# Performance work log

Measured on AMD Instinct MI355X. Metric: run time of the kernel, lower is better.

The kernel has to match this reference:

```python
import math
import jax, jax.numpy as jnp
import numpy as np

Bn, NA, NE = 16384, 15, 16
H, NH, DH = 256, 4, 64
DO, DA, DE = 30, 32, 32
NACT, BS = 6, 2048


def setup_inputs():
    key = jax.random.key(0)
    c = [0]
    def nxt():
        c[0] += 1
        return jax.random.fold_in(key, c[0])
    def nrm(shape, scale=1.0):
        return jax.random.normal(nxt(), shape, jnp.float32) * scale
    sH = 1.0 / math.sqrt(H)
    own_raw = nrm((Bn, 1, DO))
    ally_raw = nrm((Bn, NA, DA))
    enemy_raw = nrm((Bn, NE, DE))
    # zero-rows encode invisible entities (mask is derived from all-zero check)
    mA = jax.random.bernoulli(nxt(), 0.8, (Bn, NA)).at[:, 0].set(True)
    mE = jax.random.bernoulli(nxt(), 0.8, (Bn, NE)).at[:, 0].set(True)
    ally_raw = ally_raw * mA[..., None]
    enemy_raw = enemy_raw * mE[..., None]
    return dict(
        own_raw=own_raw, ally_raw=ally_raw, enemy_raw=enemy_raw,
        hidden_state=nrm((Bn, H), 0.1),
        W_own=nrm((H, DO), 1.0 / math.sqrt(DO)), b_own=jnp.zeros((H,)),
        W_ally=nrm((H, DA), 1.0 / math.sqrt(DA)), b_ally=jnp.zeros((H,)),
        W_enemy=nrm((H, DE), 1.0 / math.sqrt(DE)), b_enemy=jnp.zeros((H,)),
        gt_w=nrm((2,), 0.1), gt_b=jnp.zeros((2,)),
        attnA_W=nrm((4, H, H), sH), attnA_b=jnp.zeros((4, H)),
        attnE_W=nrm((4, H, H), sH), attnE_b=jnp.zeros((4, H)),
        clnA_W=nrm((2, H, H), 0.1 * sH), clnA_b=jnp.zeros((2, H)),
        clnE_W=nrm((2, H, H), 0.1 * sH), clnE_b=jnp.zeros((2, H)),
        ln3_g=jnp.ones((3 * H,)), ln3_b=jnp.zeros((3 * H,)),
        gru_Wih=nrm((3 * H, 3 * H), 1.0 / math.sqrt(3 * H)),
        gru_Whh=nrm((3 * H, H), sH),
        gru_bih=jnp.zeros((3 * H,)), gru_bhh=jnp.zeros((3 * H,)),
        Wv_head=nrm((1, H), sH), bv_head=jnp.zeros((1,)),
        Wtb=nrm((2, H), sH), btb=jnp.zeros((2,)),
        log_tau=jnp.zeros((2,)),
        Wmq=nrm((H, H), sH), bmq=jnp.zeros((H,)),
        prototypes=nrm((NACT, H), sH),
        Wqs=nrm((H, H), sH), bqs=jnp.zeros((H,)),
        Wke=nrm((H, H), sH), bke=jnp.zeros((H,)),
        bs=BS,
    )


def _group_temp(cnt, w, b):
    # GroupTemp: positive temperature from group cardinality
    return jax.nn.softplus(w * jnp.log1p(cnt) + b) + 1.0


def _mhga(q, K, mask, temp, W, b):
    # multi-head group attention: single query over a small entity set
    B, N, _ = K.shape
    qh = (q @ W[0].T + b[0]).reshape(B, NH, DH)
    kh = (K @ W[1].T + b[1]).reshape(B, N, NH, DH)
    vh = (K @ W[2].T + b[2]).reshape(B, N, NH, DH)
    s = jnp.einsum('bhd,bnhd->bhn', qh, kh) / math.sqrt(DH)
    s = s / temp[:, None, None]
    s = jnp.where(mask[:, None, :], s, -1e30)
    p = jax.nn.softmax(s, axis=-1)
    z = jnp.einsum('bhn,bnhd->bhd', p, vh).reshape(B, H)
    return z @ W[3].T + b[3]


def _cln(x, cond, W, b, eps=1e-5):
    # conditional LayerNorm: scale/shift predicted from own-feature embedding
    mu = x.mean(-1, keepdims=True)
    var = ((x - mu) ** 2).mean(-1, keepdims=True)
    xn = (x - mu) * jax.lax.rsqrt(var + eps)
    gamma = 1.0 + cond @ W[0].T + b[0]
    beta = cond @ W[1].T + b[1]
    return gamma * xn + beta


def _ln(x, g, b, eps=1e-5):
    mu = x.mean(-1, keepdims=True)
    var = ((x - mu) ** 2).mean(-1, keepdims=True)
    return (x - mu) * jax.lax.rsqrt(var + eps) * g + b


def reference(own_raw, ally_raw, enemy_raw, hidden_state, W_own, b_own,
              W_ally, b_ally, W_enemy, b_enemy, gt_w, gt_b,
              attnA_W, attnA_b, attnE_W, attnE_b,
              clnA_W, clnA_b, clnE_W, clnE_b, ln3_g, ln3_b,
              gru_Wih, gru_Whh, gru_bih, gru_bhh,
              Wv_head, bv_head, Wtb, btb, log_tau,
              Wmq, bmq, prototypes, Wqs, bqs, Wke, bke, bs):
    ally_mask = jnp.any(ally_raw != 0, axis=-1)     # [B,nA]
    enemy_mask = jnp.any(enemy_raw != 0, axis=-1)   # [B,nE]
    e_own = own_raw @ W_own.T + b_own               # [B,1,H]
    A = ally_raw @ W_ally.T + b_ally                # [B,nA,H]
    E = enemy_raw @ W_enemy.T + b_enemy             # [B,nE,H]
    q_src = e_own[:, 0]
    tA = _group_temp(ally_mask.sum(-1).astype(jnp.float32), gt_w[0], gt_b[0])
    tE = _group_temp(enemy_mask.sum(-1).astype(jnp.float32), gt_w[1], gt_b[1])
    zA = _cln(_mhga(q_src, A, ally_mask, tA, attnA_W, attnA_b), q_src, clnA_W, clnA_b)
    zE = _cln(_mhga(q_src, E, enemy_mask, tE, attnE_W, attnE_b), q_src, clnE_W, clnE_b)
    u = _ln(jnp.concatenate([q_src, zA, zE], axis=-1), ln3_g, ln3_b)
    # GRUCell (PyTorch gate layout: r, z, n)
    gi = u @ gru_Wih.T + gru_bih
    gh = hidden_state @ gru_Whh.T + gru_bhh
    ir, iz, inn = jnp.split(gi, 3, axis=-1)
    hr, hz, hn = jnp.split(gh, 3, axis=-1)
    r = jax.nn.sigmoid(ir + hr)
    zg = jax.nn.sigmoid(iz + hz)
    n = jnp.tanh(inn + r * hn)
    h = (1.0 - zg) * n + zg * hidden_state
    V = h @ Wv_head.T + bv_head                     # [B,1]
    tb = h @ Wtb.T + btb
    b_move, b_shoot = tb[:, 0:1], tb[:, 1:2]
    tau_move = jnp.exp(log_tau[0]) + 1e-6
    tau_shoot = jnp.exp(log_tau[1]) + 1e-6
    # prototype movement head
    q_mv = h @ Wmq.T + bmq
    A_move = q_mv @ prototypes.T / math.sqrt(H)
    A_move = A_move - A_move.mean(-1, keepdims=True)
    Q_move = V + b_move + A_move / tau_move
    # shoot pointer head over enemies
    q_sh = h @ Wqs.T + bqs
    Ke = E @ Wke.T + bke
    a = jnp.einsum('bh,bnh->bn', q_sh, Ke) / math.sqrt(H)
    emf = enemy_mask.astype(a.dtype)
    den = jnp.maximum(emf.sum(1, keepdims=True), 1.0)
    a = a - (a * emf).sum(1, keepdims=True) / den
    a = jnp.where(enemy_mask, a, -1e30)
    Q_shoot = V + b_shoot + a / tau_shoot
    Q = jnp.concatenate([Q_move, Q_shoot], axis=-1)[:, None, :]  # [B,1,NACT+nE]
    return Q, h.reshape(bs, -1, H)
```

## Files before the change

kernel.cpp:

```cpp
#include <hip/hip_runtime.h>
#include <math.h>

#define BN 16384

typedef float f32x4 __attribute__((ext_vector_type(4)));
typedef short bf16x8v __attribute__((ext_vector_type(8)));
typedef unsigned short u16x8 __attribute__((ext_vector_type(8)));
typedef unsigned short u16x4 __attribute__((ext_vector_type(4)));

static __device__ inline unsigned short f2bf(float f) {
  unsigned u = __float_as_uint(f);
  return (unsigned short)((u + 0x8000u) >> 16);
}
static __device__ inline float bf2f(unsigned short u) {
  return __uint_as_float(((unsigned)u) << 16);
}

#define XS(r) (((r) >> 1) & 3)

#define WKA_OFF   0
#define WVA_OFF   8192
#define WKE_OFF   16384
#define WVE_OFF   24576
#define WKEF_OFF  32768
#define BKA_OFF   40960
#define BVA_OFF   41216
#define BKE_OFF   41472
#define BVE_OFF   41728
#define BKEF_OFF  41984
#define WMP_OFF   43008
#define BMP_OFF   44544
#define G_OFF     45056
#define BG_OFF    53248
#define WQB_OFF   53312
#define SC0_OFF   53568
#define BMG_OFF   53632
#define CLB_OFF   53888
#define BPJA_OFF  57088
#define BPJE_OFF  57344
#define BGRU_OFF  57600
#define BHD_OFF   16384

#define QSRC_OFF  65536
#define BUF1_OFF  (QSRC_OFF + BN*256)
#define BUF2_OFF  (BUF1_OFF + BN*256)
#define BUF3_OFF  (BUF2_OFF + BN*256)
#define BUF4_OFF  (BUF3_OFF + BN*256)
#define BUF5_OFF  (BUF4_OFF + BN*256)

#define GBUF_OFF  BUF1_OFF
#define AOUTA_OFF BUF3_OFF
#define AOUTE_OFF BUF4_OFF
#define GBB_OFF   BUF5_OFF
#define UB_OFF    (BUF5_OFF + 8388608)

#define HOFF      (BN*22)

#define MGB_S 0
#define CLA_S 65536
#define CLE_S 196608
#define PJA_S 327680
#define PJE_S 360448

__global__ __launch_bounds__(256) void k_fuseA(
    const float* __restrict__ attnA_W, const float* __restrict__ attnA_b,
    const float* __restrict__ attnE_W, const float* __restrict__ attnE_b,
    const float* __restrict__ W_ally,  const float* __restrict__ b_ally,
    const float* __restrict__ W_enemy, const float* __restrict__ b_enemy,
    const float* __restrict__ Wke,     const float* __restrict__ bke,
    const float* __restrict__ clnA_W,  const float* __restrict__ clnE_W,
    float* __restrict__ FW, unsigned short* __restrict__ WBc) {
  int g = blockIdx.x * 256 + threadIdx.x;
  if (g < 40960) {
    int m = g >> 13;
    int r = g & 8191;
    int d = r >> 5, j = r & 31;
    const float *Wout, *Win, *bin, *bout; float *dst, *dstb;
    switch (m) {
      case 0: Wout = attnA_W + 65536;  Win = W_ally;  bin = b_ally;  bout = attnA_b + 256; dst = FW + WKA_OFF;  dstb = FW + BKA_OFF;  break;
      case 1: Wout = attnA_W + 131072; Win = W_ally;  bin = b_ally;  bout = attnA_b + 512; dst = FW + WVA_OFF;  dstb = FW + BVA_OFF;  break;
      case 2: Wout = attnE_W + 65536;  Win = W_enemy; bin = b_enemy; bout = attnE_b + 256; dst = FW + WKE_OFF;  dstb = FW + BKE_OFF;  break;
      case 3: Wout = attnE_W + 131072; Win = W_enemy; bin = b_enemy; bout = attnE_b + 512; dst = FW + WVE_OFF;  dstb = FW + BVE_OFF;  break;
      default:Wout = Wke;              Win = W_enemy; bin = b_enemy; bout = bke;           dst = FW + WKEF_OFF; dstb = FW + BKEF_OFF; break;
    }
    float acc = 0.f;
    for (int c = 0; c < 256; ++c) acc += Wout[d*256 + c] * Win[c*32 + j];
    dst[d*32 + j] = acc;
    if (j == 0) {
      float b = bout[d];
      for (int c = 0; c < 256; ++c) b += Wout[d*256 + c] * bin[c];
      dstb[d] = b;
    }
  } else {
    int t = g - 40960;
    if (t < 65536) {
      int e = t * 4;
      const float* src = (e < 131072) ? clnA_W : clnE_W;
      int off = (e < 131072) ? 0 : 131072;
      float4 v = *(const float4*)(src + (e - off));
      u16x4 b; b.x = f2bf(v.x); b.y = f2bf(v.y); b.z = f2bf(v.z); b.w = f2bf(v.w);
      *(u16x4*)&WBc[CLA_S + e] = b;
    }
  }
}

__global__ __launch_bounds__(256) void k_fuseB(
    const float* __restrict__ protos, const float* __restrict__ Wmq,
    const float* __restrict__ bmq,    const float* __restrict__ Wqs,
    const float* __restrict__ bqs,
    const float* __restrict__ attnA_W, const float* __restrict__ attnA_b,
    const float* __restrict__ attnE_W, const float* __restrict__ attnE_b,
    const float* __restrict__ clnA_b,  const float* __restrict__ clnE_b,
    float* __restrict__ FW, unsigned short* __restrict__ WBc) {
  int g = blockIdx.x * 256 + threadIdx.x;
  const float* WKe_f = FW + WKEF_OFF;
  const float* bKe_f = FW + BKEF_OFF;
  if (g < 10240) {
    if (g < 1536) {
      int i = g >> 8, c = g & 255;
      float acc = 0.f;
      for (int d = 0; d < 256; ++d) acc += protos[i*256 + d] * Wmq[d*256 + c];
      FW[WMP_OFF + i*256 + c] = acc;
    } else if (g < 9728) {
      int r = g - 1536;
      int j = r >> 8, c = r & 255;
      float acc = 0.f;
      for (int d = 0; d < 256; ++d) acc += WKe_f[d*32 + j] * Wqs[d*256 + c];
      FW[G_OFF + j*256 + c] = acc;
    } else if (g < 9984) {
      int c = g - 9728;
      float acc = 0.f;
      for (int d = 0; d < 256; ++d) acc += Wqs[d*256 + c] * bKe_f[d];
      FW[WQB_OFF + c] = acc;
    } else if (g < 9990) {
      int i = g - 9984;
      float acc = 0.f;
      for (int d = 0; d < 256; ++d) acc += protos[i*256 + d] * bmq[d];
      FW[BMP_OFF + i] = acc;
    } else if (g < 10022) {
      int j = g - 9990;
      float acc = 0.f;
      for (int d = 0; d < 256; ++d) acc += WKe_f[d*32 + j] * bqs[d];
      FW[BG_OFF + j] = acc;
    } else if (g == 10022) {
      float acc = 0.f;
      for (int d = 0; d < 256; ++d) acc += bqs[d] * bKe_f[d];
      FW[SC0_OFF] = acc;
    }
  } else if (g < 77056) {
    int t = g - 10240;
    if (t < 65536) {
      int r = t >> 8, c = t & 255;
      int br = r >> 7, jj = r & 127, h = jj >> 5, jc = jj & 31;
      const float* W0 = br ? attnE_W : attnA_W;
      const float* Wk = FW + (br ? WKE_OFF : WKA_OFF);
      float acc = 0.f;
      for (int d = 0; d < 64; ++d)
        acc += W0[(h*64+d)*256 + c] * Wk[(h*64+d)*32 + jc];
      WBc[MGB_S + r*256 + c] = f2bf(acc);
    } else if (t < 65792) {
      int r = t - 65536;
      int br = r >> 7, jj = r & 127, h = jj >> 5, jc = jj & 31;
      const float* b0 = br ? attnE_b : attnA_b;
      const float* Wk = FW + (br ? WKE_OFF : WKA_OFF);
      float acc = 0.f;
      for (int d = 0; d < 64; ++d) acc += b0[h*64+d] * Wk[(h*64+d)*32 + jc];
      FW[BMG_OFF + r] = acc;
    } else {
      int c = t - 65792;
      FW[CLB_OFF + c] = (c < 512) ? clnA_b[c] : clnE_b[c - 512];
    }
  } else {
    int t = g - 77056;
    if (t < 65536) {
      int br = t >> 15;
      int r0 = t & 32767;
      int o = r0 >> 7, r = r0 & 127, h = r >> 5, j = r & 31;
      const float* Wp = (br ? attnE_W : attnA_W) + 196608;
      const float* Wv = FW + (br ? WVE_OFF : WVA_OFF);
      float acc = 0.f;
      for (int d = 0; d < 64; ++d)
        acc += Wp[o*256 + h*64 + d] * Wv[(h*64+d)*32 + j];
      WBc[(br ? PJE_S : PJA_S) + o*128 + r] = f2bf(acc);
    } else if (t < 66048) {
      int r0 = t - 65536;
      int br = r0 >> 8, c = r0 & 255;
      const float* Wp = (br ? attnE_W : attnA_W) + 196608;
      const float* bv = FW + (br ? BVE_OFF : BVA_OFF);
      const float* pb = (br ? attnE_b : attnA_b) + 768;
      float acc = pb[c];
      for (int d = 0; d < 256; ++d) acc += Wp[c*256 + d] * bv[d];
      FW[(br ? BPJE_OFF : BPJA_OFF) + c] = acc;
    }
  }
}

__global__ __launch_bounds__(256) void k_fuse4(
    const float* __restrict__ Wv_head, const float* __restrict__ bv_head,
    const float* __restrict__ Wtb, const float* __restrict__ btb,
    float* __restrict__ FW, unsigned short* __restrict__ WHD) {
  int g = blockIdx.x * 256 + threadIdx.x;
  if (g < 32768) {
    int r = g >> 8, c = g & 255;
    float v;
    if (r == 0)       v = Wv_head[c];
    else if (r == 1)  v = Wtb[c];
    else if (r == 2)  v = Wtb[256 + c];
    else if (r < 9)   v = FW[WMP_OFF + (r - 3) * 256 + c];
    else if (r < 41)  v = FW[G_OFF + (r - 9) * 256 + c];
    else if (r == 41) v = FW[WQB_OFF + c];
    else              v = 0.f;
    WHD[r * 256 + c] = f2bf(v);
  } else if (g < 32896) {
    int r = g - 32768;
    float v;
    if (r == 0)       v = bv_head[0];
    else if (r == 1)  v = btb[0];
    else if (r == 2)  v = btb[1];
    else if (r < 9)   v = FW[BMP_OFF + r - 3];
    else if (r < 41)  v = FW[BG_OFF + r - 9];
    else if (r == 41) v = FW[SC0_OFF];
    else              v = 0.f;
    FW[BHD_OFF + r] = v;
  }
}

__global__ __launch_bounds__(256) void k_gruw(
    const float* __restrict__ Wih, const float* __restrict__ Whh,
    const float* __restrict__ bih, const float* __restrict__ bhh,
    unsigned short* __restrict__ WG, float* __restrict__ BG) {
  int t = blockIdx.x * 256 + threadIdx.x;
  if (t < 262144) {
    int e4 = t * 4;
    int p = e4 >> 10, c = e4 & 1023;
    int X = p >> 8, df = (p >> 6) & 3, g = (p >> 4) & 3, i = p & 15;
    int d = X * 64 + df * 16 + i;
    float4 v;
    if (c < 768) {
      if (g == 3) v = make_float4(0.f, 0.f, 0.f, 0.f);
      else        v = *(const float4*)(Wih + (long)(g * 256 + d) * 768 + c);
    } else {
      int ch = c - 768;
      if (g == 2) v = make_float4(0.f, 0.f, 0.f, 0.f);
      else {
        int row = (g == 3 ? 512 : g * 256) + d;
        v = *(const float4*)(Whh + (long)row * 256 + ch);
      }
    }
    u16x4 b; b.x = f2bf(v.x); b.y = f2bf(v.y); b.z = f2bf(v.z); b.w = f2bf(v.w);
    *(u16x4*)&WG[e4] = b;
  } else if (t < 263168) {
    int p = t - 262144;
    int X = p >> 8, df = (p >> 6) & 3, g = (p >> 4) & 3, i = p & 15;
    int d = X * 64 + df * 16 + i;
    float v;
    if (g == 0)      v = bih[d] + bhh[d];
    else if (g == 1) v = bih[256 + d] + bhh[256 + d];
    else if (g == 2) v = bih[512 + d];
    else             v = bhh[512 + d];
    BG[p] = v;
  }
}

template<int K, int NOUT>
__global__ __launch_bounds__(256) void k_densek(
    const float* __restrict__ A, const float* __restrict__ W,
    const float* __restrict__ bias, unsigned short* __restrict__ Cb) {
  constexpr int KB = 32;
  __shared__ float As[64][36];
  const int tid = threadIdx.x;
  const int s0 = blockIdx.x * 64;
  const int o0 = blockIdx.y * 64;
  const int ox = (tid & 15) * 4;
  const int sy = (tid >> 4) * 4;
  float acc[4][4] = {};
  const float* Abase = A + (long)s0 * K;
  for (int idx = tid; idx < 64 * KB; idx += 256) {
    int s = idx >> 5, c = idx & 31;
    As[s][c] = (c < K) ? Abase[(long)s * K + c] : 0.f;
  }
  __syncthreads();
  for (int kk = 0; kk < KB; kk += 4) {
    float a4[4][4];
    #pragma unroll
    for (int sj = 0; sj < 4; ++sj)
      *(float4*)a4[sj] = *(const float4*)&As[sy + sj][kk];
    #pragma unroll
    for (int oi = 0; oi < 4; ++oi) {
      float w4[4];
      #pragma unroll
      for (int kx = 0; kx < 4; ++kx) {
        int k = kk + kx;
        w4[kx] = (k < K) ? W[(long)(o0 + ox + oi) * K + k] : 0.f;
      }
      #pragma unroll
      for (int sj = 0; sj < 4; ++sj)
        #pragma unroll
        for (int kx = 0; kx < 4; ++kx)
          acc[sj][oi] = fmaf(a4[sj][kx], w4[kx], acc[sj][oi]);
    }
  }
  #pragma unroll
  for (int sj = 0; sj < 4; ++sj) {
    u16x4 b4;
    b4.x = f2bf(acc[sj][0] + bias[o0 + ox + 0]);
    b4.y = f2bf(acc[sj][1] + bias[o0 + ox + 1]);
    b4.z = f2bf(acc[sj][2] + bias[o0 + ox + 2]);
    b4.w = f2bf(acc[sj][3] + bias[o0 + ox + 3]);
    *(u16x4*)&Cb[(long)(s0 + sy + sj) * NOUT + o0 + ox] = b4;
  }
}

#define MM_PROLOG(GDX)                                                        \
  __shared__ __align__(16) unsigned short As[4096];                           \
  __shared__ __align__(16) unsigned short Ws[4096];                           \
  const int tid = threadIdx.x;                                                \
  const int pid = blockIdx.y * (GDX) + blockIdx.x;                            \
  const int bx = (pid >> 3) % (GDX);                                          \
  const int by = ((pid >> 3) / (GDX)) * 8 + (pid & 7);                        \
  const long s0 = (long)by * 128;                                             \
  const int wv = tid >> 6, l = tid & 63;                                      \
  const int wm = (wv >> 1) * 64, wn = (wv & 1) * 64;                          \
  const int lr = l & 15, lk = l >> 4;                                         \
  const int wrow = tid >> 2;                                                  \
  const int wslot = tid & 3;                                                  \
  (void)wrow; (void)wslot;                                                    \
  f32x4 acc[4][4] = {};

#define MM_MFMA_STEP                                                          \
  {                                                                           \
    bf16x8v af[4], bw[4];                                                     \
    _Pragma("unroll")                                                         \
    for (int m = 0; m < 4; ++m) {                                             \
      const int r = wm + m * 16 + lr;                                         \
      af[m] = *(const bf16x8v*)&As[r * 32 + ((lk ^ XS(r)) * 8)];              \
    }                                                                         \
    _Pragma("unroll")                                                         \
    for (int n = 0; n < 4; ++n) {                                             \
      const int r = wn + n * 16 + lr;                                         \
      bw[n] = *(const bf16x8v*)&Ws[r * 32 + ((lk ^ XS(r)) * 8)];              \
    }                                                                         \
    _Pragma("unroll")                                                         \
    for (int m = 0; m < 4; ++m)                                               \
      _Pragma("unroll")                                                       \
      for (int n = 0; n < 4; ++n)                                             \
        acc[m][n] = __builtin_amdgcn_mfma_f32_16x16x32_bf16(af[m], bw[n], acc[m][n], 0, 0, 0); \
  }

__global__ __launch_bounds__(256) void k_mm_qs(
    const unsigned short* __restrict__ Abf, const unsigned short* __restrict__ W,
    const float* __restrict__ bias, unsigned short* __restrict__ Cg,
    unsigned short* __restrict__ Cgb) {
  MM_PROLOG(10)
  const int o0 = bx * 128;
  u16x8 pw[2], pa_b[2];
  const unsigned short* Wb = W + (long)o0 * 256;
  #pragma unroll
  for (int p = 0; p < 2; ++p) {
    const int r = wrow + 64 * p;
    pw[p]   = *(const u16x8*)(Wb + (long)r * 256 + wslot * 8);
    pa_b[p] = *(const u16x8*)(Abf + (s0 + r) * 256 + wslot * 8);
  }
  for (int ch = 0; ch < 8; ++ch) {
    if (ch) __syncthreads();
    #pragma unroll
    for (int p = 0; p < 2; ++p) {
      const int r = wrow + 64 * p;
      const int ps = (wslot ^ XS(r)) * 8;
      *(u16x8*)&Ws[r * 32 + ps] = pw[p];
      *(u16x8*)&As[r * 32 + ps] = pa_b[p];
    }
    __syncthreads();
    if (ch + 1 < 8) {
      const int k0 = (ch + 1) * 32;
      #pragma unroll
      for (int p = 0; p < 2; ++p) {
        const int r = wrow + 64 * p;
        pw[p]   = *(const u16x8*)(Wb + (long)r * 256 + k0 + wslot * 8);
        pa_b[p] = *(const u16x8*)(Abf + (s0 + r) * 256 + k0 + wslot * 8);
      }
    }
    MM_MFMA_STEP
  }
  if (bx < 2) {
    const int ob = bx * 128;
    #pragma unroll
    for (int n = 0; n < 4; ++n) {
      const float b = bias[o0 + wn + n * 16 + lr];
      #pragma unroll
      for (int m = 0; m < 4; ++m) {
        const long rowb = s0 + wm + m * 16 + lk * 4;
        #pragma unroll
        for (int r = 0; r < 4; ++r)
          Cg[(rowb + r) * 256 + ob + wn + n * 16 + lr] = f2bf(acc[m][n][r] + b);
      }
    }
  } else {
    const int ob = (bx - 2) * 128;
    #pragma unroll
    for (int n = 0; n < 4; ++n) {
      const float b = bias[o0 + wn + n * 16 + lr];
      #pragma unroll
      for (int m = 0; m < 4; ++m) {
        const long rowb = s0 + wm + m * 16 + lk * 4;
        #pragma unroll
        for (int r = 0; r < 4; ++r)
          Cgb[(rowb + r) * 1024 + ob + wn + n * 16 + lr] = f2bf(acc[m][n][r] + b);
      }
    }
  }
}

__global__ __launch_bounds__(256) void k_mm_pv(
    const unsigned short* __restrict__ pal, const unsigned short* __restrict__ W,
    const float* __restrict__ bias, unsigned short* __restrict__ CA,
    unsigned short* __restrict__ CE) {
  MM_PROLOG(4)
  const int o0 = bx * 128;
  const int br = bx >> 1;
  const unsigned short* Abf = pal + br * 128;
  u16x8 pw[2], pa_b[2];
  const unsigned short* Wb = W + (long)o0 * 128;
  #pragma unroll
  for (int p = 0; p < 2; ++p) {
    const int r = wrow + 64 * p;
    pw[p]   = *(const u16x8*)(Wb + (long)r * 128 + wslot * 8);
    pa_b[p] = *(const u16x8*)(Abf + (s0 + r) * 256 + wslot * 8);
  }
  for (int ch = 0; ch < 4; ++ch) {
    if (ch) __syncthreads();
    #pragma unroll
    for (int p = 0; p < 2; ++p) {
      const int r = wrow + 64 * p;
      const int ps = (wslot ^ XS(r)) * 8;
      *(u16x8*)&Ws[r * 32 + ps] = pw[p];
      *(u16x8*)&As[r * 32 + ps] = pa_b[p];
    }
    __syncthreads();
    if (ch + 1 < 4) {
      const int k0 = (ch + 1) * 32;
      #pragma unroll
      for (int p = 0; p < 2; ++p) {
        const int r = wrow + 64 * p;
        pw[p]   = *(const u16x8*)(Wb + (long)r * 128 + k0 + wslot * 8);
        pa_b[p] = *(const u16x8*)(Abf + (s0 + r) * 256 + k0 + wslot * 8);
      }
    }
    MM_MFMA_STEP
  }
  unsigned short* C = br ? CE : CA;
  const int ob = (bx & 1) * 128;
  #pragma unroll
  for (int n = 0; n < 4; ++n) {
    const float b = bias[o0 + wn + n * 16 + lr];
    #pragma unroll
    for (int m = 0; m < 4; ++m) {
      const long rowb = s0 + wm + m * 16 + lk * 4;
      #pragma unroll
      for (int r = 0; r < 4; ++r)
        C[(rowb + r) * 256 + ob + wn + n * 16 + lr] = f2bf(acc[m][n][r] + b);
    }
  }
}

__global__ __launch_bounds__(512, 4) void k_gru6(
    const unsigned short* __restrict__ UB, const float* __restrict__ hid,
    const unsigned short* __restrict__ WG, const float* __restrict__ BG,
    float* __restrict__ hout) {
  __shared__ __align__(16) unsigned short As[4096];
  __shared__ __align__(16) unsigned short Ws[8192];
  const int tid = threadIdx.x;
  const int pid = blockIdx.y * 4 + blockIdx.x;
  const int lin = pid >> 3;
  const int bx = lin & 3;
  const int by = (lin >> 2) * 8 + (pid & 7);
  const long s0 = (long)by * 128;
  const int wv = tid >> 6, l = tid & 63;
  const int sh = wv >> 2;
  const int cq = wv & 3;
  const int lr = l & 15, lk = l >> 4;
  const int row = tid >> 2;
  const int q = tid & 3;

  f32x4 acc[4][4] = {};
  u16x8 pw[2], pa_b;
  float4 pa_f[2];

  const unsigned short* Wb = WG + (long)(bx * 256) * 1024;

  pw[0] = *(const u16x8*)(Wb + (long)row * 1024 + q * 8);
  pw[1] = *(const u16x8*)(Wb + (long)(row + 128) * 1024 + q * 8);
  pa_b = *(const u16x8*)(UB + (s0 + row) * 768 + q * 8);

#define GRU6_MFMA(SKIPG)                                                      \
  {                                                                           \
    bf16x8v af[4], bw[4];                                                     \
    _Pragma("unroll")                                                         \
    for (int m = 0; m < 4; ++m) {                                             \
      const int r = sh * 64 + m * 16 + lr;                                    \
      af[m] = *(const bf16x8v*)&As[r * 32 + ((lk ^ XS(r)) * 8)];              \
    }                                                                         \
    _Pragma("unroll")                                                         \
    for (int n = 0; n < 4; ++n) {                                             \
      const int r = cq * 64 + n * 16 + lr;                                    \
      bw[n] = *(const bf16x8v*)&Ws[r * 32 + ((lk ^ XS(r)) * 8)];              \
    }                                                                         \
    _Pragma("unroll")                                                         \
    for (int m = 0; m < 4; ++m)                                               \
      _Pragma("unroll")                                                       \
      for (int n = 0; n < 4; ++n)                                             \
        if (n != (SKIPG))                                                     \
          acc[m][n] = __builtin_amdgcn_mfma_f32_16x16x32_bf16(af[m], bw[n], acc[m][n], 0, 0, 0); \
  }

  for (int ch = 0; ch < 24; ++ch) {
    if (ch) __syncthreads();
    {
      *(u16x8*)&Ws[row * 32 + ((q ^ XS(row)) * 8)] = pw[0];
      const int r1 = row + 128;
      *(u16x8*)&Ws[r1 * 32 + ((q ^ XS(r1)) * 8)] = pw[1];
      *(u16x8*)&As[row * 32 + ((q ^ XS(row)) * 8)] = pa_b;
    }
    __syncthreads();
    {
      const int k0 = (ch + 1) * 32;
      pw[0] = *(const u16x8*)(Wb + (long)row * 1024 + k0 + q * 8);
      pw[1] = *(const u16x8*)(Wb + (long)(row + 128) * 1024 + k0 + q * 8);
      if (ch + 1 < 24) {
        pa_b = *(const u16x8*)(UB + (s0 + row) * 768 + k0 + q * 8);
      } else {
        const float* Af = hid + (s0 + row) * 256 + q * 8;
        pa_f[0] = *(const float4*)(Af);
        pa_f[1] = *(const float4*)(Af + 4);
      }
    }
    GRU6_MFMA(3)
  }
  for (int ch = 24; ch < 32; ++ch) {
    __syncthreads();
    {
      *(u16x8*)&Ws[row * 32 + ((q ^ XS(row)) * 8)] = pw[0];
      const int r1 = row + 128;
      *(u16x8*)&Ws[r1 * 32 + ((q ^ XS(r1)) * 8)] = pw[1];
      float fa[8];
      *(float4*)&fa[0] = pa_f[0];
      *(float4*)&fa[4] = pa_f[1];
      u16x8 pk;
      #pragma unroll
      for (int i = 0; i < 8; ++i) pk[i] = f2bf(fa[i]);
      *(u16x8*)&As[row * 32 + ((q ^ XS(row)) * 8)] = pk;
    }
    __syncthreads();
    if (ch + 1 < 32) {
      const int k0 = (ch + 1) * 32;
      const int km = k0 - 768;
      pw[0] = *(const u16x8*)(Wb + (long)row * 1024 + k0 + q * 8);
      pw[1] = *(const u16x8*)(Wb + (long)(row + 128) * 1024 + k0 + q * 8);
      const float* Af = hid + (s0 + row) * 256 + km + q * 8;
      pa_f[0] = *(const float4*)(Af);
      pa_f[1] = *(const float4*)(Af + 4);
    }
    GRU6_MFMA(2)
  }

  const int d = bx * 64 + cq * 16 + lr;
  const int bb = bx * 256 + cq * 64 + lr;
  const float bR  = BG[bb];
  const float bZ  = BG[bb + 16];
  const float bNi = BG[bb + 32];
  const float bNh = BG[bb + 48];
  #pragma unroll
  for (int m = 0; m < 4; ++m) {
    const long srow = s0 + sh * 64 + m * 16 + lk * 4;
    #pragma unroll
    for (int rr = 0; rr < 4; ++rr) {
      const long s = srow + rr;
      const float r_ = 1.f / (1.f + expf(-(acc[m][0][rr] + bR)));
      const float z_ = 1.f / (1.f + expf(-(acc[m][1][rr] + bZ)));
      const float n_ = tanhf(acc[m][2][rr] + bNi + r_ * (acc[m][3][rr] + bNh));
      const float hp = hid[s * 256 + d];
      hout[s * 256 + d] = (1.f - z_) * n_ + z_ * hp;
    }
  }
#undef GRU6_MFMA
}

__global__ __launch_bounds__(256) void k_core2(
    const float* __restrict__ rawA, const float* __restrict__ rawE,
    const unsigned short* __restrict__ g, const float* __restrict__ gt_w,
    const float* __restrict__ gt_b, unsigned short* __restrict__ pal) {
  __shared__ float A_[4][15][36];
  __shared__ float E_[4][16][36];
  __shared__ float G_[4][8][32];
  __shared__ float P_[4][8][16];
  const int tid = threadIdx.x;
  const int w = tid >> 6, l = tid & 63;
  const long s = (long)blockIdx.x * 4 + w;

  const float* ra = rawA + s * 480;
  const float* re = rawE + s * 512;
  const unsigned short* gr = g + s * 256;
  #pragma unroll
  for (int i = l; i < 120; i += 64) {
    float4 v = *(const float4*)(ra + i * 4);
    *(float4*)&A_[w][i >> 3][(i & 7) * 4] = v;
  }
  #pragma unroll
  for (int i = l; i < 128; i += 64) {
    float4 v = *(const float4*)(re + i * 4);
    *(float4*)&E_[w][i >> 3][(i & 7) * 4] = v;
  }
  {
    u16x4 v = *(const u16x4*)(gr + l * 4);
    float4 f = { bf2f(v.x), bf2f(v.y), bf2f(v.z), bf2f(v.w) };
    *(float4*)&G_[w][l >> 3][(l & 7) * 4] = f;
  }
  __syncthreads();

  bool mv = false;
  if (l < 15) {
    #pragma unroll
    for (int c = 0; c < 8; ++c) {
      float4 x = *(const float4*)&A_[w][l][c * 4];
      mv |= (x.x != 0.f) | (x.y != 0.f) | (x.z != 0.f) | (x.w != 0.f);
    }
  } else if (l >= 16 && l < 32) {
    #pragma unroll
    for (int c = 0; c < 8; ++c) {
      float4 x = *(const float4*)&E_[w][l - 16][c * 4];
      mv |= (x.x != 0.f) | (x.y != 0.f) | (x.z != 0.f) | (x.w != 0.f);
    }
  }
  unsigned long long bal = __ballot(mv);
  unsigned mA = (unsigned)bal & 0x7FFFu;
  unsigned mE = (unsigned)(bal >> 16) & 0xFFFFu;
  float xa = gt_w[0] * log1pf((float)__popc(mA)) + gt_b[0];
  float spa = fmaxf(xa, 0.f) + log1pf(expf(-fabsf(xa)));
  float scaleA = 1.f / (8.f * (spa + 1.f));
  float xe = gt_w[1] * log1pf((float)__popc(mE)) + gt_b[1];
  float spe = fmaxf(xe, 0.f) + log1pf(expf(-fabsf(xe)));
  float scaleE = 1.f / (8.f * (spe + 1.f));

  {
    const int h = l >> 4, n = l & 15;
    const bool okA = (n < 15) && ((mA >> n) & 1);
    const bool okE = (mE >> n) & 1;
    const float* arow = &A_[w][n < 15 ? n : 0][0];
    const float* erow = &E_[w][n][0];
    const float* garow = &G_[w][h][0];
    const float* gerow = &G_[w][4 + h][0];
    float accA = 0.f, accE = 0.f;
    #pragma unroll
    for (int j = 0; j < 32; ++j) {
      accA = fmaf(garow[j], arow[j], accA);
      accE = fmaf(gerow[j], erow[j], accE);
    }
    float sA = okA ? accA * scaleA : -INFINITY;
    float sE = okE ? accE * scaleE : -INFINITY;
    float mAx = sA, mEx = sE;
    #pragma unroll
    for (int off = 8; off; off >>= 1) {
      mAx = fmaxf(mAx, __shfl_xor(mAx, off));
      mEx = fmaxf(mEx, __shfl_xor(mEx, off));
    }
    float eA = okA ? expf(sA - mAx) : 0.f;
    float eE = okE ? expf(sE - mEx) : 0.f;
    float suA = eA, suE = eE;
    #pragma unroll
    for (int off = 8; off; off >>= 1) {
      suA += __shfl_xor(suA, off);
      suE += __shfl_xor(suE, off);
    }
    P_[w][h][n] = eA / suA;
    P_[w][4 + h][n] = eE / suE;
  }
  __syncthreads();

  {
    const int j = l & 31, hh = l >> 5;
    unsigned short* po = pal + s * 256 + hh * 32 + j;
    #pragma unroll
    for (int r = 0; r < 2; ++r) {
      const int ha = r * 2 + hh;
      float a0 = 0.f, a1 = 0.f;
      #pragma unroll
      for (int n = 0; n < 15; ++n)
        a0 = fmaf(P_[w][ha][n], A_[w][n][j], a0);
      #pragma unroll
      for (int n = 0; n < 16; ++n)
        a1 = fmaf(P_[w][4 + ha][n], E_[w][n][j], a1);
      po[r * 64] = f2bf(a0);
      po[128 + r * 64] = f2bf(a1);
    }
  }
}

__global__ __launch_bounds__(256) void k_clnln(
    const unsigned short* __restrict__ aA, const unsigned short* __restrict__ aE,
    const unsigned short* __restrict__ qsb, const unsigned short* __restrict__ gbb,
    const float* __restrict__ g, const float* __restrict__ b,
    unsigned short* __restrict__ UB) {
  int w = threadIdx.x >> 6, l = threadIdx.x & 63;
  long s = (long)blockIdx.x * 4 + w;
  int d = l * 4;
  u16x4 av = *(const u16x4*)(aA + s * 256 + d);
  u16x4 ev = *(const u16x4*)(aE + s * 256 + d);
  u16x4 qv = *(const u16x4*)(qsb + s * 256 + d);
  float4 vA = { bf2f(av.x), bf2f(av.y), bf2f(av.z), bf2f(av.w) };
  float4 vE = { bf2f(ev.x), bf2f(ev.y), bf2f(ev.z), bf2f(ev.w) };
  float4 vq = { bf2f(qv.x), bf2f(qv.y), bf2f(qv.z), bf2f(qv.w) };
  const unsigned short* gbr = gbb + s * 1024;
  float sumA = vA.x + vA.y + vA.z + vA.w;
  float ssqA = vA.x*vA.x + vA.y*vA.y + vA.z*vA.z + vA.w*vA.w;
  float sumE = vE.x + vE.y + vE.z + vE.w;
  float ssqE = vE.x*vE.x + vE.y*vE.y + vE.z*vE.z + vE.w*vE.w;
  #pragma unroll
  for (int off = 32; off > 0; off >>= 1) {
    sumA += __shfl_xor(sumA, off); ssqA += __shfl_xor(ssqA, off);
    sumE += __shfl_xor(sumE, off); ssqE += __shfl_xor(ssqE, off);
  }
  float muA = sumA * (1.f / 256.f);
  float rstdA = rsqrtf(ssqA * (1.f / 256.f) - muA * muA + 1e-5f);
  float muE = sumE * (1.f / 256.f);
  float rstdE = rsqrtf(ssqE * (1.f / 256.f) - muE * muE + 1e-5f);

  u16x4 u0 = *(const u16x4*)(gbr + d);
  u16x4 u1 = *(const u16x4*)(gbr + 256 + d);
  u16x4 u2 = *(const u16x4*)(gbr + 512 + d);
  u16x4 u3 = *(const u16x4*)(gbr + 768 + d);
  float4 gA4 = { bf2f(u0.x), bf2f(u0.y), bf2f(u0.z), bf2f(u0.w) };
  float4 bA4 = { bf2f(u1.x), bf2f(u1.y), bf2f(u1.z), bf2f(u1.w) };
  float4 gE4 = { bf2f(u2.x), bf2f(u2.y), bf2f(u2.z), bf2f(u2.w) };
  float4 bE4 = { bf2f(u3.x), bf2f(u3.y), bf2f(u3.z), bf2f(u3.w) };
  float4 zA, zE;
  zA.x = (1.f + gA4.x) * ((vA.x - muA) * rstdA) + bA4.x;
  zA.y = (1.f + gA4.y) * ((vA.y - muA) * rstdA) + bA4.y;
  zA.z = (1.f + gA4.z) * ((vA.z - muA) * rstdA) + bA4.z;
  zA.w = (1.f + gA4.w) * ((vA.w - muA) * rstdA) + bA4.w;
  zE.x = (1.f + gE4.x) * ((vE.x - muE) * rstdE) + bE4.x;
  zE.y = (1.f + gE4.y) * ((vE.y - muE) * rstdE) + bE4.y;
  zE.z = (1.f + gE4.z) * ((vE.z - muE) * rstdE) + bE4.z;
  zE.w = (1.f + gE4.w) * ((vE.w - muE) * rstdE) + bE4.w;

  float sum = vq.x+vq.y+vq.z+vq.w + zA.x+zA.y+zA.z+zA.w + zE.x+zE.y+zE.z+zE.w;
  float ssq = vq.x*vq.x+vq.y*vq.y+vq.z*vq.z+vq.w*vq.w
            + zA.x*zA.x+zA.y*zA.y+zA.z*zA.z+zA.w*zA.w
            + zE.x*zE.x+zE.y*zE.y+zE.z*zE.z+zE.w*zE.w;
  #pragma unroll
  for (int off = 32; off > 0; off >>= 1) {
    sum += __shfl_xor(sum, off); ssq += __shfl_xor(ssq, off);
  }
  float mu = sum * (1.f / 768.f);
  float rstd = rsqrtf(ssq * (1.f / 768.f) - mu * mu + 1e-5f);

  float4 g0 = *(const float4*)(g + d),       b0 = *(const float4*)(b + d);
  float4 g1 = *(const float4*)(g + 256 + d), b1 = *(const float4*)(b + 256 + d);
  float4 g2 = *(const float4*)(g + 512 + d), b2 = *(const float4*)(b + 512 + d);
  unsigned short* ur = UB + s * 768;
  u16x4 o;
  o.x = f2bf((vq.x - mu) * rstd * g0.x + b0.x);
  o.y = f2bf((vq.y - mu) * rstd * g0.y + b0.y);
  o.z = f2bf((vq.z - mu) * rstd * g0.z + b0.z);
  o.w = f2bf((vq.w - mu) * rstd * g0.w + b0.w);
  *(u16x4*)&ur[d] = o;
  o.x = f2bf((zA.x - mu) * rstd * g1.x + b1.x);
  o.y = f2bf((zA.y - mu) * rstd * g1.y + b1.y);
  o.z = f2bf((zA.z - mu) * rstd * g1.z + b1.z);
  o.w = f2bf((zA.w - mu) * rstd * g1.w + b1.w);
  *(u16x4*)&ur[256 + d] = o;
  o.x = f2bf((zE.x - mu) * rstd * g2.x + b2.x);
  o.y = f2bf((zE.y - mu) * rstd * g2.y + b2.y);
  o.z = f2bf((zE.z - mu) * rstd * g2.z + b2.z);
  o.w = f2bf((zE.w - mu) * rstd * g2.w + b2.w);
  *(u16x4*)&ur[512 + d] = o;
}

__global__ __launch_bounds__(256) void k_headsmm(
    const float* __restrict__ h, const unsigned short* __restrict__ WHD,
    const float* __restrict__ BHD, const float* __restrict__ eraw,
    const float* __restrict__ log_tau, float* __restrict__ Qout) {
  __shared__ __align__(16) unsigned short As[2048];
  __shared__ __align__(16) unsigned short Ws[2048];
  __shared__ float obs[64][49];
  const int tid = threadIdx.x;
  const long s0 = (long)blockIdx.x * 64;
  const int wv = tid >> 6, l = tid & 63;
  const int lr = l & 15, lk = l >> 4;
  const int row = tid >> 2;
  const int q = tid & 3;
  f32x4 acc[4] = {};
  u16x8 pw;
  float4 pa_f[2];
  pw = *(const u16x8*)(WHD + (long)row * 256 + q * 8);
  {
    const float* Af = h + (s0 + row) * 256 + q * 8;
    pa_f[0] = *(const float4*)(Af);
    pa_f[1] = *(const float4*)(Af + 4);
  }
  for (int ch = 0; ch < 8; ++ch) {
    if (ch) __syncthreads();
    *(u16x8*)&Ws[row * 32 + ((q ^ XS(row)) * 8)] = pw;
    {
      float fa[8];
      *(float4*)&fa[0] = pa_f[0];
      *(float4*)&fa[4] = pa_f[1];
      u16x8 pk;
      #pragma unroll
      for (int i = 0; i < 8; ++i) pk[i] = f2bf(fa[i]);
      *(u16x8*)&As[row * 32 + ((q ^ XS(row)) * 8)] = pk;
    }
    __syncthreads();
    if (ch + 1 < 8) {
      const int k0 = (ch + 1) * 32;
      pw = *(const u16x8*)(WHD + (long)row * 256 + k0 + q * 8);
      const float* Af = h + (s0 + row) * 256 + k0 + q * 8;
      pa_f[0] = *(const float4*)(Af);
      pa_f[1] = *(const float4*)(Af + 4);
    }
    {
      bf16x8v af, bw[4];
      {
        const int r = wv * 16 + lr;
        af = *(const bf16x8v*)&As[r * 32 + ((lk ^ XS(r)) * 8)];
      }
      #pragma unroll
      for (int n = 0; n < 4; ++n) {
        const int r = n * 16 + lr;
        bw[n] = *(const bf16x8v*)&Ws[r * 32 + ((lk ^ XS(r)) * 8)];
      }
      #pragma unroll
      for (int n = 0; n < 4; ++n)
        acc[n] = __builtin_amdgcn_mfma_f32_16x16x32_bf16(af, bw[n], acc[n], 0, 0, 0);
    }
  }
  #pragma unroll
  for (int n = 0; n < 3; ++n) {
    const int col = n * 16 + lr;
    const float b = BHD[col];
    const int rowo = wv * 16 + lk * 4;
    #pragma unroll
    for (int rr = 0; rr < 4; ++rr)
      obs[rowo + rr][col] = acc[n][rr] + b;
  }
  __syncthreads();
  const float itm = 1.f / (expf(log_tau[0]) + 1e-6f);
  const float its = 1.f / (expf(log_tau[1]) + 1e-6f);
  for (int rep = 0; rep < 4; ++rep) {
    const int sloc = rep * 16 + (tid >> 4);
    const int i = tid & 15;
    const long s = s0 + sloc;
    const float V = obs[sloc][0];
    const float* er = eraw + s * 512 + i * 32;
    bool valid = false; float a0 = 0.f;
    #pragma unroll
    for (int jb = 0; jb < 8; ++jb) {
      float4 e4 = *(const float4*)(er + jb * 4);
      valid |= (e4.x != 0.f) | (e4.y != 0.f) | (e4.z != 0.f) | (e4.w != 0.f);
      a0 += obs[sloc][9 + jb * 4 + 0] * e4.x + obs[sloc][9 + jb * 4 + 1] * e4.y +
            obs[sloc][9 + jb * 4 + 2] * e4.z + obs[sloc][9 + jb * 4 + 3] * e4.w;
    }
    float a = (a0 + obs[sloc][41]) * 0.0625f;
    float sa = valid ? a : 0.f;
    float cv = valid ? 1.f : 0.f;
    #pragma unroll
    for (int off = 8; off > 0; off >>= 1) {
      sa += __shfl_xor(sa, off);
      cv += __shfl_xor(cv, off);
    }
    float me = sa / fmaxf(cv, 1.f);
    Qout[s * 22 + 6 + i] = V + obs[sloc][2] + (valid ? (a - me) * its : -1e30f * its);
    if (i < 6) {
      float mean = 0.f;
      #pragma unroll
      for (int t = 0; t < 6; ++t) mean += obs[sloc][3 + t];
      mean *= (1.f / 6.f);
      Qout[s * 22 + i] = V + obs[sloc][1] + (obs[sloc][3 + i] - mean) * 0.0625f * itm;
    }
  }
}

extern "C" void kernel_launch(void* const* d_in, const int* in_sizes, int n_in,
                              void* d_out, int out_size, void* d_ws, size_t ws_size,
                              hipStream_t stream) {
  const float* own_raw   = (const float*)d_in[0];
  const float* ally_raw  = (const float*)d_in[1];
  const float* enemy_raw = (const float*)d_in[2];
  const float* hidden    = (const float*)d_in[3];
  const float* W_own     = (const float*)d_in[4];
  const float* b_own     = (const float*)d_in[5];
  const float* W_ally    = (const float*)d_in[6];
  const float* b_ally    = (const float*)d_in[7];
  const float* W_enemy   = (const float*)d_in[8];
  const float* b_enemy   = (const float*)d_in[9];
  const float* gt_w      = (const float*)d_in[10];
  const float* gt_b      = (const float*)d_in[11];
  const float* attnA_W   = (const float*)d_in[12];
  const float* attnA_b   = (const float*)d_in[13];
  const float* attnE_W   = (const float*)d_in[14];
  const float* attnE_b   = (const float*)d_in[15];
  const float* clnA_W    = (const float*)d_in[16];
  const float* clnA_b    = (const float*)d_in[17];
  const float* clnE_W    = (const float*)d_in[18];
  const float* clnE_b    = (const float*)d_in[19];
  const float* ln3_g     = (const float*)d_in[20];
  const float* ln3_b     = (const float*)d_in[21];
  const float* gru_Wih   = (const float*)d_in[22];
  const float* gru_Whh   = (const float*)d_in[23];
  const float* gru_bih   = (const float*)d_in[24];
  const float* gru_bhh   = (const float*)d_in[25];
  const float* Wv_head   = (const float*)d_in[26];
  const float* bv_head   = (const float*)d_in[27];
  const float* Wtb       = (const float*)d_in[28];
  const float* btb       = (const float*)d_in[29];
  const float* log_tau   = (const float*)d_in[30];
  const float* Wmq       = (const float*)d_in[31];
  const float* bmq       = (const float*)d_in[32];
  const float* protos    = (const float*)d_in[33];
  const float* Wqs       = (const float*)d_in[34];
  const float* bqs       = (const float*)d_in[35];
  const float* Wke       = (const float*)d_in[36];
  const float* bke       = (const float*)d_in[37];

  float* ws  = (float*)d_ws;
  float* out = (float*)d_out;
  float* hout = out + HOFF;
  unsigned short* WB   = (unsigned short*)hout;
  unsigned short* qsb  = (unsigned short*)(ws + BUF2_OFF);
  unsigned short* palb = (unsigned short*)(ws + QSRC_OFF);
  unsigned short* WHD  = (unsigned short*)ws;
  unsigned short* wgru = (unsigned short*)(ws + BUF1_OFF);
  unsigned short* gb16 = (unsigned short*)(ws + GBUF_OFF);
  unsigned short* aoA  = (unsigned short*)(ws + AOUTA_OFF);
  unsigned short* aoE  = (unsigned short*)(ws + AOUTE_OFF);
  unsigned short* gbb  = (unsigned short*)(ws + GBB_OFF);
  unsigned short* ub   = (unsigned short*)(ws + UB_OFF);

  k_fuseA<<<416, 256, 0, stream>>>(attnA_W, attnA_b, attnE_W, attnE_b,
                                   W_ally, b_ally, W_enemy, b_enemy, Wke, bke,
                                   clnA_W, clnE_W, ws, WB);
  k_fuseB<<<559, 256, 0, stream>>>(protos, Wmq, bmq, Wqs, bqs,
                                   attnA_W, attnA_b, attnE_W, attnE_b,
                                   clnA_b, clnE_b, ws, WB);
  k_fuse4<<<129, 256, 0, stream>>>(Wv_head, bv_head, Wtb, btb, ws, WHD);

  k_densek<30, 256><<<dim3(BN/64, 4), 256, 0, stream>>>(own_raw, W_own, b_own, qsb);

  k_mm_qs<<<dim3(10, 128), 256, 0, stream>>>(qsb, WB, ws + BMG_OFF, gb16, gbb);

  k_core2<<<BN/4, 256, 0, stream>>>(ally_raw, enemy_raw, gb16, gt_w, gt_b, palb);

  k_gruw<<<1028, 256, 0, stream>>>(gru_Wih, gru_Whh, gru_bih, gru_bhh,
                                   wgru, ws + BGRU_OFF);

  k_mm_pv<<<dim3(4, 128), 256, 0, stream>>>(palb, WB + PJA_S, ws + BPJA_OFF,
                                            aoA, aoE);

  k_clnln<<<BN/4, 256, 0, stream>>>(aoA, aoE, qsb, gbb, ln3_g, ln3_b, ub);

  k_gru6<<<dim3(4, 128), 512, 0, stream>>>(ub, hidden, wgru, ws + BGRU_OFF, hout);

  k_headsmm<<<BN/64, 256, 0, stream>>>(hout, WHD, ws + BHD_OFF, enemy_raw,
                                       log_tau, out);
}
```

Before: 181.7 us.

## Double-buffer GRU GEMM shared tiles and split weight-fusion dot products across threads

The GRU GEMM kernel now keeps two LDS buffers for both A and W tiles. Each chunk's MFMA work runs on the current buffer while the next chunk is written into the other, so one barrier per iteration is removed. Separately, the weight-folding kernels k_fuseA and k_fuseB split each 256-length dot product between two threads and combine the halves with a shuffle. This doubles the thread count to shorten the serial loops. The cost is double the LDS in the GRU kernel, which could lower occupancy, plus extra shuffles and idle lanes on the writes.

After: 178.8 us. About the same (-1.6%).

```diff
diff --git a/kernel.cpp b/kernel.cpp
--- a/kernel.cpp
+++ b/kernel.cpp
@@ -71,9 +71,10 @@
     const float* __restrict__ clnA_W,  const float* __restrict__ clnE_W,
     float* __restrict__ FW, unsigned short* __restrict__ WBc) {
   int g = blockIdx.x * 256 + threadIdx.x;
-  if (g < 40960) {
-    int m = g >> 13;
-    int r = g & 8191;
+  if (g < 81920) {
+    int u = g >> 1, t = g & 1;
+    int m = u >> 13;
+    int r = u & 8191;
     int d = r >> 5, j = r & 31;
     const float *Wout, *Win, *bin, *bout; float *dst, *dstb;
     switch (m) {
@@ -83,16 +84,19 @@
       case 3: Wout = attnE_W + 131072; Win = W_enemy; bin = b_enemy; bout = attnE_b + 512; dst = FW + WVE_OFF;  dstb = FW + BVE_OFF;  break;
       default:Wout = Wke;              Win = W_enemy; bin = b_enemy; bout = bke;           dst = FW + WKEF_OFF; dstb = FW + BKEF_OFF; break;
     }
+    const int c0 = t * 128;
     float acc = 0.f;
-    for (int c = 0; c < 256; ++c) acc += Wout[d*256 + c] * Win[c*32 + j];
-    dst[d*32 + j] = acc;
+    for (int c = c0; c < c0 + 128; ++c) acc += Wout[d*256 + c] * Win[c*32 + j];
+    acc += __shfl_xor(acc, 1);
+    if (t == 0) dst[d*32 + j] = acc;
     if (j == 0) {
-      float b = bout[d];
-      for (int c = 0; c < 256; ++c) b += Wout[d*256 + c] * bin[c];
-      dstb[d] = b;
+      float b = 0.f;
+      for (int c = c0; c < c0 + 128; ++c) b += Wout[d*256 + c] * bin[c];
+      b += __shfl_xor(b, 1);
+      if (t == 0) dstb[d] = b + bout[d];
     }
   } else {
-    int t = g - 40960;
+    int t = g - 81920;
     if (t < 65536) {
       int e = t * 4;
       const float* src = (e < 131072) ? clnA_W : clnE_W;
@@ -115,40 +119,48 @@
   int g = blockIdx.x * 256 + threadIdx.x;
   const float* WKe_f = FW + WKEF_OFF;
   const float* bKe_f = FW + BKEF_OFF;
-  if (g < 10240) {
-    if (g < 1536) {
-      int i = g >> 8, c = g & 255;
+  if (g < 20480) {
+    int u = g >> 1, tt = g & 1;
+    const int c0 = tt * 128;
+    if (u < 1536) {
+      int i = u >> 8, c = u & 255;
       float acc = 0.f;
-      for (int d = 0; d < 256; ++d) acc += protos[i*256 + d] * Wmq[d*256 + c];
-      FW[WMP_OFF + i*256 + c] = acc;
-    } else if (g < 9728) {
-      int r = g - 1536;
+      for (int d = c0; d < c0 + 128; ++d) acc += protos[i*256 + d] * Wmq[d*256 + c];
+      acc += __shfl_xor(acc, 1);
+      if (tt == 0) FW[WMP_OFF + i*256 + c] = acc;
+    } else if (u < 9728) {
+      int r = u - 1536;
       int j = r >> 8, c = r & 255;
       float acc = 0.f;
-      for (int d = 0; d < 256; ++d) acc += WKe_f[d*32 + j] * Wqs[d*256 + c];
-      FW[G_OFF + j*256 + c] = acc;
-    } else if (g < 9984) {
-      int c = g - 9728;
+      for (int d = c0; d < c0 + 128; ++d) acc += WKe_f[d*32 + j] * Wqs[d*256 + c];
+      acc += __shfl_xor(acc, 1);
+      if (tt == 0) FW[G_OFF + j*256 + c] = acc;
+    } else if (u < 9984) {
+      int c = u - 9728;
       float acc = 0.f;
-      for (int d = 0; d < 256; ++d) acc += Wqs[d*256 + c] * bKe_f[d];
-      FW[WQB_OFF + c] = acc;
-    } else if (g < 9990) {
-      int i = g - 9984;
+      for (int d = c0; d < c0 + 128; ++d) acc += Wqs[d*256 + c] * bKe_f[d];
+      acc += __shfl_xor(acc, 1);
+      if (tt == 0) FW[WQB_OFF + c] = acc;
+    } else if (u < 9990) {
+      int i = u - 9984;
       float acc = 0.f;
-      for (int d = 0; d < 256; ++d) acc += protos[i*256 + d] * bmq[d];
-      FW[BMP_OFF + i] = acc;
-    } else if (g < 10022) {
-      int j = g - 9990;
+      for (int d = c0; d < c0 + 128; ++d) acc += protos[i*256 + d] * bmq[d];
+      acc += __shfl_xor(acc, 1);
+      if (tt == 0) FW[BMP_OFF + i] = acc;
+    } else if (u < 10022) {
+      int j = u - 9990;
       float acc = 0.f;
-      for (int d = 0; d < 256; ++d) acc += WKe_f[d*32 + j] * bqs[d];
-      FW[BG_OFF + j] = acc;
-    } else if (g == 10022) {
+      for (int d = c0; d < c0 + 128; ++d) acc += WKe_f[d*32 + j] * bqs[d];
+      acc += __shfl_xor(acc, 1);
+      if (tt == 0) FW[BG_OFF + j] = acc;
+    } else if (u == 10022) {
       float acc = 0.f;
-      for (int d = 0; d < 256; ++d) acc += bqs[d] * bKe_f[d];
-      FW[SC0_OFF] = acc;
-    }
-  } else if (g < 77056) {
-    int t = g - 10240;
+      for (int d = c0; d < c0 + 128; ++d) acc += bqs[d] * bKe_f[d];
+      acc += __shfl_xor(acc, 1);
+      if (tt == 0) FW[SC0_OFF] = acc;
+    }
+  } else if (g < 87296) {
+    int t = g - 20480;
     if (t < 65536) {
       int r = t >> 8, c = t & 255;
       int br = r >> 7, jj = r & 127, h = jj >> 5, jc = jj & 31;
@@ -171,7 +183,7 @@
       FW[CLB_OFF + c] = (c < 512) ? clnA_b[c] : clnE_b[c - 512];
     }
   } else {
-    int t = g - 77056;
+    int t = g - 87296;
     if (t < 65536) {
       int br = t >> 15;
       int r0 = t & 32767;
@@ -463,12 +475,12 @@
   }
 }
 
-__global__ __launch_bounds__(512, 4) void k_gru6(
+__global__ __launch_bounds__(512, 4) void k_gru7(
     const unsigned short* __restrict__ UB, const float* __restrict__ hid,
     const unsigned short* __restrict__ WG, const float* __restrict__ BG,
     float* __restrict__ hout) {
-  __shared__ __align__(16) unsigned short As[4096];
-  __shared__ __align__(16) unsigned short Ws[8192];
+  __shared__ __align__(16) unsigned short As[2][4096];
+  __shared__ __align__(16) unsigned short Ws[2][8192];
   const int tid = threadIdx.x;
   const int pid = blockIdx.y * 4 + blockIdx.x;
   const int lin = pid >> 3;
@@ -488,22 +500,20 @@
 
   const unsigned short* Wb = WG + (long)(bx * 256) * 1024;
 
-  pw[0] = *(const u16x8*)(Wb + (long)row * 1024 + q * 8);
-  pw[1] = *(const u16x8*)(Wb + (long)(row + 128) * 1024 + q * 8);
-  pa_b = *(const u16x8*)(UB + (s0 + row) * 768 + q * 8);
-
-#define GRU6_MFMA(SKIPG)                                                      \
+#define GRU7_MFMA(CUR, SKIPG)                                                 \
   {                                                                           \
+    const unsigned short* AsC = As[CUR];                                      \
+    const unsigned short* WsC = Ws[CUR];                                      \
     bf16x8v af[4], bw[4];                                                     \
     _Pragma("unroll")                                                         \
     for (int m = 0; m < 4; ++m) {                                             \
       const int r = sh * 64 + m * 16 + lr;                                    \
-      af[m] = *(const bf16x8v*)&As[r * 32 + ((lk ^ XS(r)) * 8)];              \
+      af[m] = *(const bf16x8v*)&AsC[r * 32 + ((lk ^ XS(r)) * 8)];             \
     }                                                                         \
     _Pragma("unroll")                                                         \
     for (int n = 0; n < 4; ++n) {                                             \
       const int r = cq * 64 + n * 16 + lr;                                    \
-      bw[n] = *(const bf16x8v*)&Ws[r * 32 + ((lk ^ XS(r)) * 8)];              \
+      bw[n] = *(const bf16x8v*)&WsC[r * 32 + ((lk ^ XS(r)) * 8)];             \
     }                                                                         \
     _Pragma("unroll")                                                         \
     for (int m = 0; m < 4; ++m)                                               \
@@ -513,15 +523,23 @@
           acc[m][n] = __builtin_amdgcn_mfma_f32_16x16x32_bf16(af[m], bw[n], acc[m][n], 0, 0, 0); \
   }
 
+#define GRU7_STAGE_W(BUF)                                                     \
+  {                                                                           \
+    unsigned short* WsN = Ws[BUF];                                            \
+    *(u16x8*)&WsN[row * 32 + ((q ^ XS(row)) * 8)] = pw[0];                    \
+    const int r1 = row + 128;                                                 \
+    *(u16x8*)&WsN[r1 * 32 + ((q ^ XS(r1)) * 8)] = pw[1];                      \
+  }
+
+  pw[0] = *(const u16x8*)(Wb + (long)row * 1024 + q * 8);
+  pw[1] = *(const u16x8*)(Wb + (long)(row + 128) * 1024 + q * 8);
+  pa_b = *(const u16x8*)(UB + (s0 + row) * 768 + q * 8);
+  GRU7_STAGE_W(0)
+  *(u16x8*)&As[0][row * 32 + ((q ^ XS(row)) * 8)] = pa_b;
+  __syncthreads();
+
   for (int ch = 0; ch < 24; ++ch) {
-    if (ch) __syncthreads();
-    {
-      *(u16x8*)&Ws[row * 32 + ((q ^ XS(row)) * 8)] = pw[0];
-      const int r1 = row + 128;
-      *(u16x8*)&Ws[r1 * 32 + ((q ^ XS(r1)) * 8)] = pw[1];
-      *(u16x8*)&As[row * 32 + ((q ^ XS(row)) * 8)] = pa_b;
-    }
-    __syncthreads();
+    const int cur = ch & 1;
     {
       const int k0 = (ch + 1) * 32;
       pw[0] = *(const u16x8*)(Wb + (long)row * 1024 + k0 + q * 8);
@@ -534,23 +552,23 @@
         pa_f[1] = *(const float4*)(Af + 4);
       }
     }
-    GRU6_MFMA(3)
-  }
-  for (int ch = 24; ch < 32; ++ch) {
-    __syncthreads();
-    {
-      *(u16x8*)&Ws[row * 32 + ((q ^ XS(row)) * 8)] = pw[0];
-      const int r1 = row + 128;
-      *(u16x8*)&Ws[r1 * 32 + ((q ^ XS(r1)) * 8)] = pw[1];
+    GRU7_MFMA(cur, 3)
+    GRU7_STAGE_W(cur ^ 1)
+    if (ch + 1 < 24) {
+      *(u16x8*)&As[cur ^ 1][row * 32 + ((q ^ XS(row)) * 8)] = pa_b;
+    } else {
       float fa[8];
       *(float4*)&fa[0] = pa_f[0];
       *(float4*)&fa[4] = pa_f[1];
       u16x8 pk;
       #pragma unroll
       for (int i = 0; i < 8; ++i) pk[i] = f2bf(fa[i]);
-      *(u16x8*)&As[row * 32 + ((q ^ XS(row)) * 8)] = pk;
+      *(u16x8*)&As[cur ^ 1][row * 32 + ((q ^ XS(row)) * 8)] = pk;
     }
     __syncthreads();
+  }
+  for (int ch = 24; ch < 32; ++ch) {
+    const int cur = ch & 1;
     if (ch + 1 < 32) {
       const int k0 = (ch + 1) * 32;
       const int km = k0 - 768;
@@ -560,7 +578,18 @@
       pa_f[0] = *(const float4*)(Af);
       pa_f[1] = *(const float4*)(Af + 4);
     }
-    GRU6_MFMA(2)
+    GRU7_MFMA(cur, 2)
+    if (ch + 1 < 32) {
+      GRU7_STAGE_W(cur ^ 1)
+      float fa[8];
+      *(float4*)&fa[0] = pa_f[0];
+      *(float4*)&fa[4] = pa_f[1];
+      u16x8 pk;
+      #pragma unroll
+      for (int i = 0; i < 8; ++i) pk[i] = f2bf(fa[i]);
+      *(u16x8*)&As[cur ^ 1][row * 32 + ((q ^ XS(row)) * 8)] = pk;
+      __syncthreads();
+    }
   }
 
   const int d = bx * 64 + cq * 16 + lr;
@@ -582,7 +611,8 @@
       hout[s * 256 + d] = (1.f - z_) * n_ + z_ * hp;
     }
   }
-#undef GRU6_MFMA
+#undef GRU7_MFMA
+#undef GRU7_STAGE_W
 }
 
 __global__ __launch_bounds__(256) void k_core2(
@@ -935,10 +965,10 @@
   unsigned short* gbb  = (unsigned short*)(ws + GBB_OFF);
   unsigned short* ub   = (unsigned short*)(ws + UB_OFF);
 
-  k_fuseA<<<416, 256, 0, stream>>>(attnA_W, attnA_b, attnE_W, attnE_b,
+  k_fuseA<<<576, 256, 0, stream>>>(attnA_W, attnA_b, attnE_W, attnE_b,
                                    W_ally, b_ally, W_enemy, b_enemy, Wke, bke,
                                    clnA_W, clnE_W, ws, WB);
-  k_fuseB<<<559, 256, 0, stream>>>(protos, Wmq, bmq, Wqs, bqs,
+  k_fuseB<<<599, 256, 0, stream>>>(protos, Wmq, bmq, Wqs, bqs,
                                    attnA_W, attnA_b, attnE_W, attnE_b,
                                    clnA_b, clnE_b, ws, WB);
   k_fuse4<<<129, 256, 0, stream>>>(Wv_head, bv_head, Wtb, btb, ws, WHD);
@@ -957,7 +987,7 @@
 
   k_clnln<<<BN/4, 256, 0, stream>>>(aoA, aoE, qsb, gbb, ln3_g, ln3_b, ub);
 
-  k_gru6<<<dim3(4, 128), 512, 0, stream>>>(ub, hidden, wgru, ws + BGRU_OFF, hout);
+  k_gru7<<<dim3(4, 128), 512, 0, stream>>>(ub, hidden, wgru, ws + BGRU_OFF, hout);
 
   k_headsmm<<<BN/64, 256, 0, stream>>>(hout, WHD, ws + BHD_OFF, enemy_raw,
                                        log_tau, out);
```
